# Kernel optimization log

Measured on AMD Instinct MI355X. Metric: run time of the kernel, lower is better.

The kernel has to match this reference:

```python
import jax, jax.numpy as jnp
import numpy as np

H = 16  # num_heads

def setup_inputs() -> dict:
    key = jax.random.key(0)
    ks = jax.random.split(key, 9)
    B, S, D = 4, 1024, 1024
    s = 0.02
    return {
        "x": jax.random.normal(ks[0], (B, S, D), jnp.float32),
        "Wq": jax.random.normal(ks[1], (D, D), jnp.float32) * s,
        "bq": jax.random.normal(ks[2], (D,), jnp.float32) * s,
        "Wk": jax.random.normal(ks[3], (D, D), jnp.float32) * s,
        "bk": jax.random.normal(ks[4], (D,), jnp.float32) * s,
        "Wv": jax.random.normal(ks[5], (D, D), jnp.float32) * s,
        "bv": jax.random.normal(ks[6], (D,), jnp.float32) * s,
        "Wo": jax.random.normal(ks[7], (D, D), jnp.float32) * s,
        "bo": jax.random.normal(ks[8], (D,), jnp.float32) * s,
    }

def reference(x, Wq, bq, Wk, bk, Wv, bv, Wo, bo):
    B, S, D = x.shape
    hd = D // H
    # Batched equivalent of the per-head Linear loop: project then split into heads.
    def proj(W, b):
        return (x @ W + b).reshape(B, S, H, hd).transpose(0, 2, 1, 3)  # [B,H,S,hd]
    q, k, v = proj(Wq, bq), proj(Wk, bk), proj(Wv, bv)
    scores = jnp.einsum("bhqd,bhkd->bhqk", q, k) / jnp.sqrt(jnp.float32(hd))
    probs = jax.nn.softmax(scores, axis=-1)  # [B,H,S,S] (dropout p=0 -> identity)
    ctx = jnp.einsum("bhqk,bhkd->bhqd", probs, v)  # [B,H,S,hd]
    ctx = ctx.transpose(0, 2, 1, 3).reshape(B, S, D)  # concat heads
    out = ctx @ Wo + bo
    return out, probs
```

## Files before the change

kernel.cpp:

```cpp
#include <hip/hip_runtime.h>
#include <math.h>

typedef unsigned short u16;
typedef __attribute__((ext_vector_type(8))) short short8;
typedef __attribute__((ext_vector_type(4))) float f32x4;

#define BB 4
#define SS 1024
#define DD 1024
#define NH 16
#define HD 64
#define BH 64

__device__ __forceinline__ u16 f2bf(float f) {
    union { float f; unsigned u; } v;
    v.f = f;
    unsigned r = v.u + 0x7fffu + ((v.u >> 16) & 1u);
    return (u16)(r >> 16);
}

__device__ __forceinline__ void gll16(const void* g, void* l) {
    __builtin_amdgcn_global_load_lds((__attribute__((address_space(1))) void*)g,
                                     (__attribute__((address_space(3))) void*)l, 16, 0, 0);
}

__global__ void cast_bf16(const float* __restrict__ X, u16* __restrict__ Y) {
    const int i = blockIdx.x * blockDim.x + threadIdx.x;
    const float4 v = reinterpret_cast<const float4*>(X)[i];
    ushort4 o;
    o.x = f2bf(v.x); o.y = f2bf(v.y); o.z = f2bf(v.z); o.w = f2bf(v.w);
    reinterpret_cast<ushort4*>(Y)[i] = o;
}

__global__ void transpose_cast_w(const float* __restrict__ W0, const float* __restrict__ W1,
                                 const float* __restrict__ W2, const float* __restrict__ W3,
                                 u16* __restrict__ O0, u16* __restrict__ O1,
                                 u16* __restrict__ O2, u16* __restrict__ O3) {
    __shared__ float T[64][65];
    const int z = blockIdx.z;
    const float* W = (z == 0) ? W0 : (z == 1) ? W1 : (z == 2) ? W2 : W3;
    u16* O = (z == 0) ? O0 : (z == 1) ? O1 : (z == 2) ? O2 : O3;
    const int k0 = blockIdx.x * 64, n0 = blockIdx.y * 64;
    const int x = threadIdx.x & 63, yq = threadIdx.x >> 6;
#pragma unroll
    for (int r = 0; r < 16; r++) {
        const int row = yq * 16 + r;
        T[row][x] = W[(size_t)(k0 + row) * 1024 + n0 + x];
    }
    __syncthreads();
#pragma unroll
    for (int r = 0; r < 16; r++) {
        const int row = yq * 16 + r;
        O[(size_t)(n0 + row) * 1024 + k0 + x] = f2bf(T[x][row]);
    }
}

__global__ void transpose_v(const u16* __restrict__ V, u16* __restrict__ VT) {
    __shared__ u16 T[64][66];
    const int t0 = blockIdx.x * 64;
    const size_t hbase = (size_t)blockIdx.y * (SS * HD);
    const int x = threadIdx.x & 63, yq = threadIdx.x >> 6;
#pragma unroll
    for (int r = 0; r < 16; r++) {
        const int trow = yq * 16 + r;
        T[trow][x] = V[hbase + (size_t)(t0 + trow) * 64 + x];
    }
    __syncthreads();
#pragma unroll
    for (int r = 0; r < 16; r++) {
        const int drow = yq * 16 + r;
        VT[hbase + (size_t)drow * 1024 + t0 + x] = T[x][drow];
    }
}

template <int MODE, int QKV>
__global__ __launch_bounds__(256) void mfma_gemm(
    const u16* __restrict__ A,
    const u16* __restrict__ Bt0, const u16* __restrict__ Bt1, const u16* __restrict__ Bt2,
    const float* __restrict__ bias0, const float* __restrict__ bias1, const float* __restrict__ bias2,
    void* __restrict__ out0, void* __restrict__ out1, void* __restrict__ out2) {
    __shared__ __align__(16) u16 As[128][32];
    __shared__ __align__(16) u16 Bs[128][32];

    const u16* Bt = Bt0;
    const float* bias = bias0;
    void* out = out0;
    if (QKV) {
        const int z = blockIdx.z;
        Bt = (z == 0) ? Bt0 : (z == 1) ? Bt1 : Bt2;
        bias = (z == 0) ? bias0 : (z == 1) ? bias1 : bias2;
        out = (z == 0) ? out0 : (z == 1) ? out1 : out2;
    }

    const int tid = threadIdx.x;
    const int w = tid >> 6, lane = tid & 63, l15 = lane & 15, quad = lane >> 4;
    const int wr = w >> 1, wc = w & 1;
    const int m0 = blockIdx.y * 128, n0 = blockIdx.x * 128;

    const u16* Ag = A + (size_t)(m0 + (tid >> 2)) * 1024 + (tid & 3) * 8;
    const u16* Bg = Bt + (size_t)(n0 + (tid >> 2)) * 1024 + (tid & 3) * 8;

    f32x4 acc[4][4];
#pragma unroll
    for (int i = 0; i < 4; i++)
#pragma unroll
        for (int j = 0; j < 4; j++) acc[i][j] = (f32x4){0.f, 0.f, 0.f, 0.f};

    for (int k0 = 0; k0 < 1024; k0 += 32) {
#pragma unroll
        for (int i = 0; i < 2; i++) {
            gll16(Ag + (size_t)(i * 64) * 1024 + k0, &As[i * 64 + w * 16][0]);
            gll16(Bg + (size_t)(i * 64) * 1024 + k0, &Bs[i * 64 + w * 16][0]);
        }
        __syncthreads();
        short8 af[4], bf[4];
#pragma unroll
        for (int i = 0; i < 4; i++)
            af[i] = *(const short8*)(&As[wr * 64 + i * 16 + l15][quad * 8]);
#pragma unroll
        for (int j = 0; j < 4; j++)
            bf[j] = *(const short8*)(&Bs[wc * 64 + j * 16 + l15][quad * 8]);
#pragma unroll
        for (int i = 0; i < 4; i++)
#pragma unroll
            for (int j = 0; j < 4; j++)
                acc[i][j] = __builtin_amdgcn_mfma_f32_16x16x32_bf16(af[i], bf[j], acc[i][j], 0, 0, 0);
        __syncthreads();
    }

#pragma unroll
    for (int i = 0; i < 4; i++) {
#pragma unroll
        for (int j = 0; j < 4; j++) {
            const int nn = n0 + wc * 64 + j * 16 + l15;
            const float bb = bias[nn];
#pragma unroll
            for (int r = 0; r < 4; r++) {
                const int mm = m0 + wr * 64 + i * 16 + quad * 4 + r;
                const float val = acc[i][j][r] + bb;
                if (MODE == 0) {
                    const int b = mm >> 10, s = mm & 1023, h = nn >> 6, d = nn & 63;
                    ((u16*)out)[((size_t)(b * NH + h) * SS + s) * HD + d] = f2bf(val);
                } else {
                    ((float*)out)[(size_t)mm * 1024 + nn] = val;
                }
            }
        }
    }
}

__global__ __launch_bounds__(256) void attn_fused(
    const u16* __restrict__ Qg, const u16* __restrict__ Kg, const u16* __restrict__ VTg,
    float* __restrict__ probs, u16* __restrict__ ctx) {
    __shared__ __align__(16) u16 Ks[2][2][64][32];
    __shared__ __align__(16) u16 Vs[2][2][64][32];
    __shared__ __align__(16) u16 Ps[4][2][16][32];

    const int tid = threadIdx.x;
    const int w = tid >> 6, lane = tid & 63, l15 = lane & 15, quad = lane >> 4;
    const int s0 = blockIdx.x * 64;
    const int bh = blockIdx.y;
    const size_t hbase = (size_t)bh * (SS * HD);

    const int qg = s0 + w * 16 + l15;
    const short8 bq0 = *(const short8*)(Qg + hbase + (size_t)qg * 64 + quad * 8);
    const short8 bq1 = *(const short8*)(Qg + hbase + (size_t)qg * 64 + 32 + quad * 8);

    float l_i = 0.f;
    {
        short8 akA[8], akB[8];
        auto loadK = [&](short8* ak, int kt) {
#pragma unroll
            for (int c = 0; c < 4; c++) {
                const u16* kr = Kg + hbase + (size_t)(kt * 64 + c * 16 + l15) * 64 + quad * 8;
                ak[c * 2] = *(const short8*)kr;
                ak[c * 2 + 1] = *(const short8*)(kr + 32);
            }
        };
        auto stats = [&](const short8* ak) {
            f32x4 sc[4];
#pragma unroll
            for (int c = 0; c < 4; c++) {
                f32x4 z = {0.f, 0.f, 0.f, 0.f};
                z = __builtin_amdgcn_mfma_f32_16x16x32_bf16(ak[c * 2], bq0, z, 0, 0, 0);
                z = __builtin_amdgcn_mfma_f32_16x16x32_bf16(ak[c * 2 + 1], bq1, z, 0, 0, 0);
                sc[c] = z;
            }
            float ss = 0.f;
#pragma unroll
            for (int c = 0; c < 4; c++)
#pragma unroll
                for (int r = 0; r < 4; r++) ss += __expf(sc[c][r] * 0.125f);
            ss += __shfl_xor(ss, 16);
            ss += __shfl_xor(ss, 32);
            l_i += ss;
        };
        loadK(akA, 0);
#pragma unroll 1
        for (int kt = 0; kt < 16; kt += 2) {
            loadK(akB, kt + 1);
            stats(akA);
            if (kt + 2 < 16) loadK(akA, kt + 2);
            stats(akB);
        }
    }
    const float linv = 1.0f / l_i;

    f32x4 oacc[4];
#pragma unroll
    for (int j = 0; j < 4; j++) oacc[j] = (f32x4){0.f, 0.f, 0.f, 0.f};

    const size_t prow = ((size_t)bh * SS + qg) * SS;

    auto stage = [&](int buf, int kt) {
#pragma unroll
        for (int i = 0; i < 2; i++) {
            const int c = i * 256 + tid;
            const int ks = c >> 8, row = (c >> 2) & 63, ch = c & 3;
            const int cb = i * 256 + (tid & ~63);
            gll16(Kg + hbase + (size_t)(kt * 64 + row) * 64 + ks * 32 + ch * 8,
                  &Ks[buf][0][0][0] + (size_t)cb * 8);
            gll16(VTg + hbase + (size_t)row * 1024 + kt * 64 + ks * 32 + ch * 8,
                  &Vs[buf][0][0][0] + (size_t)cb * 8);
        }
    };

    stage(0, 0);
    asm volatile("s_waitcnt vmcnt(0)" ::: "memory");
    __builtin_amdgcn_s_barrier();

#pragma unroll 1
    for (int kt = 0; kt < 16; kt++) {
        const int cur = kt & 1;
        if (kt < 15) stage(cur ^ 1, kt + 1);

        f32x4 sc[4];
#pragma unroll
        for (int c = 0; c < 4; c++) {
            const short8 ak0 = *(const short8*)(&Ks[cur][0][c * 16 + l15][quad * 8]);
            const short8 ak1 = *(const short8*)(&Ks[cur][1][c * 16 + l15][quad * 8]);
            f32x4 z = {0.f, 0.f, 0.f, 0.f};
            z = __builtin_amdgcn_mfma_f32_16x16x32_bf16(ak0, bq0, z, 0, 0, 0);
            z = __builtin_amdgcn_mfma_f32_16x16x32_bf16(ak1, bq1, z, 0, 0, 0);
            sc[c] = z;
        }
#pragma unroll
        for (int c = 0; c < 4; c++) {
            float p[4];
            f32x4 pv;
#pragma unroll
            for (int r = 0; r < 4; r++) {
                p[r] = __expf(sc[c][r] * 0.125f) * linv;
                pv[r] = p[r];
            }
            *(f32x4*)(probs + prow + kt * 64 + c * 16 + quad * 4) = pv;
            uint2 pk;
            pk.x = (unsigned)f2bf(p[0]) | ((unsigned)f2bf(p[1]) << 16);
            pk.y = (unsigned)f2bf(p[2]) | ((unsigned)f2bf(p[3]) << 16);
            *(uint2*)(&Ps[w][c >> 1][l15][(c & 1) * 16 + quad * 4]) = pk;
        }
        const short8 ap0 = *(const short8*)(&Ps[w][0][l15][quad * 8]);
        const short8 ap1 = *(const short8*)(&Ps[w][1][l15][quad * 8]);
#pragma unroll
        for (int j = 0; j < 4; j++) {
            const short8 bv0 = *(const short8*)(&Vs[cur][0][j * 16 + l15][quad * 8]);
            const short8 bv1 = *(const short8*)(&Vs[cur][1][j * 16 + l15][quad * 8]);
            oacc[j] = __builtin_amdgcn_mfma_f32_16x16x32_bf16(ap0, bv0, oacc[j], 0, 0, 0);
            oacc[j] = __builtin_amdgcn_mfma_f32_16x16x32_bf16(ap1, bv1, oacc[j], 0, 0, 0);
        }
        asm volatile("s_waitcnt vmcnt(0)" ::: "memory");
        __builtin_amdgcn_s_barrier();
    }

    const int b = bh >> 4, h = bh & 15;
#pragma unroll
    for (int j = 0; j < 4; j++)
#pragma unroll
        for (int r = 0; r < 4; r++) {
            const int s = s0 + w * 16 + quad * 4 + r;
            ctx[((size_t)b * SS + s) * DD + h * HD + j * 16 + l15] = f2bf(oacc[j][r]);
        }
}

extern "C" void kernel_launch(void* const* d_in, const int* in_sizes, int n_in,
                              void* d_out, int out_size, void* d_ws, size_t ws_size,
                              hipStream_t stream) {
    const float* x  = (const float*)d_in[0];
    const float* Wq = (const float*)d_in[1];
    const float* bq = (const float*)d_in[2];
    const float* Wk = (const float*)d_in[3];
    const float* bk = (const float*)d_in[4];
    const float* Wv = (const float*)d_in[5];
    const float* bv = (const float*)d_in[6];
    const float* Wo = (const float*)d_in[7];
    const float* bo = (const float*)d_in[8];

    float* out   = (float*)d_out;
    float* probs = out + (size_t)BB * SS * DD;

    char* ws = (char*)d_ws;
    u16* xb   = (u16*)(ws);
    u16* Wtq  = (u16*)(ws + (8ull << 20));
    u16* Wtk  = (u16*)(ws + (10ull << 20));
    u16* Wtv  = (u16*)(ws + (12ull << 20));
    u16* Wto  = (u16*)(ws + (14ull << 20));
    u16* qb   = (u16*)(ws + (16ull << 20));
    u16* kb   = (u16*)(ws + (24ull << 20));
    u16* vb   = (u16*)(ws + (32ull << 20));
    u16* vTb  = (u16*)(ws + (40ull << 20));
    u16* ctxb = (u16*)(ws + (48ull << 20));

    const dim3 blk(256);

    cast_bf16<<<dim3(4096), blk, 0, stream>>>(x, xb);
    transpose_cast_w<<<dim3(16, 16, 4), blk, 0, stream>>>(Wq, Wk, Wv, Wo, Wtq, Wtk, Wtv, Wto);

    mfma_gemm<0, 1><<<dim3(8, 32, 3), blk, 0, stream>>>(
        xb, Wtq, Wtk, Wtv, bq, bk, bv, qb, kb, vb);

    transpose_v<<<dim3(16, 64), blk, 0, stream>>>(vb, vTb);

    attn_fused<<<dim3(16, 64), blk, 0, stream>>>(qb, kb, vTb, probs, ctxb);

    mfma_gemm<1, 0><<<dim3(8, 32), blk, 0, stream>>>(
        ctxb, Wto, nullptr, nullptr, bo, nullptr, nullptr, out, nullptr, nullptr);
}
```

Measured before the change: 488.3 us.

## Narrow GEMM tiles, LDS-staged softmax stats pass, setprio around MFMA

```diff
diff --git a/kernel.cpp b/kernel.cpp
--- a/kernel.cpp
+++ b/kernel.cpp
@@ -80,7 +80,7 @@
     const float* __restrict__ bias0, const float* __restrict__ bias1, const float* __restrict__ bias2,
     void* __restrict__ out0, void* __restrict__ out1, void* __restrict__ out2) {
     __shared__ __align__(16) u16 As[128][32];
-    __shared__ __align__(16) u16 Bs[128][32];
+    __shared__ __align__(16) u16 Bs[64][32];
 
     const u16* Bt = Bt0;
     const float* bias = bias0;
@@ -95,44 +95,48 @@
     const int tid = threadIdx.x;
     const int w = tid >> 6, lane = tid & 63, l15 = lane & 15, quad = lane >> 4;
     const int wr = w >> 1, wc = w & 1;
-    const int m0 = blockIdx.y * 128, n0 = blockIdx.x * 128;
-
-    const u16* Ag = A + (size_t)(m0 + (tid >> 2)) * 1024 + (tid & 3) * 8;
-    const u16* Bg = Bt + (size_t)(n0 + (tid >> 2)) * 1024 + (tid & 3) * 8;
-
-    f32x4 acc[4][4];
+    const int m0 = blockIdx.y * 128, n0 = blockIdx.x * 64;
+
+    f32x4 acc[4][2];
 #pragma unroll
     for (int i = 0; i < 4; i++)
 #pragma unroll
-        for (int j = 0; j < 4; j++) acc[i][j] = (f32x4){0.f, 0.f, 0.f, 0.f};
-
+        for (int j = 0; j < 2; j++) acc[i][j] = (f32x4){0.f, 0.f, 0.f, 0.f};
+
+    const int srow = tid >> 2, sch = tid & 3;
     for (int k0 = 0; k0 < 1024; k0 += 32) {
 #pragma unroll
         for (int i = 0; i < 2; i++) {
-            gll16(Ag + (size_t)(i * 64) * 1024 + k0, &As[i * 64 + w * 16][0]);
-            gll16(Bg + (size_t)(i * 64) * 1024 + k0, &Bs[i * 64 + w * 16][0]);
-        }
+            const int c = i * 256 + tid;
+            const int row = c >> 2, ch = c & 3;
+            const int cb = i * 256 + (tid & ~63);
+            gll16(A + (size_t)(m0 + row) * 1024 + k0 + ch * 8, &As[0][0] + (size_t)cb * 8);
+        }
+        gll16(Bt + (size_t)(n0 + srow) * 1024 + k0 + sch * 8,
+              &Bs[0][0] + (size_t)(tid & ~63) * 8);
         __syncthreads();
-        short8 af[4], bf[4];
+        short8 af[4], bf[2];
 #pragma unroll
         for (int i = 0; i < 4; i++)
             af[i] = *(const short8*)(&As[wr * 64 + i * 16 + l15][quad * 8]);
 #pragma unroll
-        for (int j = 0; j < 4; j++)
-            bf[j] = *(const short8*)(&Bs[wc * 64 + j * 16 + l15][quad * 8]);
+        for (int j = 0; j < 2; j++)
+            bf[j] = *(const short8*)(&Bs[wc * 32 + j * 16 + l15][quad * 8]);
+        __builtin_amdgcn_s_setprio(1);
 #pragma unroll
         for (int i = 0; i < 4; i++)
 #pragma unroll
-            for (int j = 0; j < 4; j++)
+            for (int j = 0; j < 2; j++)
                 acc[i][j] = __builtin_amdgcn_mfma_f32_16x16x32_bf16(af[i], bf[j], acc[i][j], 0, 0, 0);
+        __builtin_amdgcn_s_setprio(0);
         __syncthreads();
     }
 
 #pragma unroll
     for (int i = 0; i < 4; i++) {
 #pragma unroll
-        for (int j = 0; j < 4; j++) {
-            const int nn = n0 + wc * 64 + j * 16 + l15;
+        for (int j = 0; j < 2; j++) {
+            const int nn = n0 + wc * 32 + j * 16 + l15;
             const float bb = bias[nn];
 #pragma unroll
             for (int r = 0; r < 4; r++) {
@@ -166,53 +170,8 @@
     const short8 bq0 = *(const short8*)(Qg + hbase + (size_t)qg * 64 + quad * 8);
     const short8 bq1 = *(const short8*)(Qg + hbase + (size_t)qg * 64 + 32 + quad * 8);
 
-    float l_i = 0.f;
-    {
-        short8 akA[8], akB[8];
-        auto loadK = [&](short8* ak, int kt) {
-#pragma unroll
-            for (int c = 0; c < 4; c++) {
-                const u16* kr = Kg + hbase + (size_t)(kt * 64 + c * 16 + l15) * 64 + quad * 8;
-                ak[c * 2] = *(const short8*)kr;
-                ak[c * 2 + 1] = *(const short8*)(kr + 32);
-            }
-        };
-        auto stats = [&](const short8* ak) {
-            f32x4 sc[4];
-#pragma unroll
-            for (int c = 0; c < 4; c++) {
-                f32x4 z = {0.f, 0.f, 0.f, 0.f};
-                z = __builtin_amdgcn_mfma_f32_16x16x32_bf16(ak[c * 2], bq0, z, 0, 0, 0);
-                z = __builtin_amdgcn_mfma_f32_16x16x32_bf16(ak[c * 2 + 1], bq1, z, 0, 0, 0);
-                sc[c] = z;
-            }
-            float ss = 0.f;
-#pragma unroll
-            for (int c = 0; c < 4; c++)
-#pragma unroll
-                for (int r = 0; r < 4; r++) ss += __expf(sc[c][r] * 0.125f);
-            ss += __shfl_xor(ss, 16);
-            ss += __shfl_xor(ss, 32);
-            l_i += ss;
-        };
-        loadK(akA, 0);
-#pragma unroll 1
-        for (int kt = 0; kt < 16; kt += 2) {
-            loadK(akB, kt + 1);
-            stats(akA);
-            if (kt + 2 < 16) loadK(akA, kt + 2);
-            stats(akB);
-        }
-    }
-    const float linv = 1.0f / l_i;
-
-    f32x4 oacc[4];
-#pragma unroll
-    for (int j = 0; j < 4; j++) oacc[j] = (f32x4){0.f, 0.f, 0.f, 0.f};
-
-    const size_t prow = ((size_t)bh * SS + qg) * SS;
-
-    auto stage = [&](int buf, int kt) {
+    const int sks = tid >> 6 >= 0 ? 0 : 0;
+    auto stageK = [&](int buf, int kt) {
 #pragma unroll
         for (int i = 0; i < 2; i++) {
             const int c = i * 256 + tid;
@@ -220,21 +179,64 @@
             const int cb = i * 256 + (tid & ~63);
             gll16(Kg + hbase + (size_t)(kt * 64 + row) * 64 + ks * 32 + ch * 8,
                   &Ks[buf][0][0][0] + (size_t)cb * 8);
+        }
+    };
+    auto stageV = [&](int buf, int kt) {
+#pragma unroll
+        for (int i = 0; i < 2; i++) {
+            const int c = i * 256 + tid;
+            const int ks = c >> 8, row = (c >> 2) & 63, ch = c & 3;
+            const int cb = i * 256 + (tid & ~63);
             gll16(VTg + hbase + (size_t)row * 1024 + kt * 64 + ks * 32 + ch * 8,
                   &Vs[buf][0][0][0] + (size_t)cb * 8);
         }
     };
 
-    stage(0, 0);
+    float l_i = 0.f;
+    stageK(0, 0);
     asm volatile("s_waitcnt vmcnt(0)" ::: "memory");
     __builtin_amdgcn_s_barrier();
-
 #pragma unroll 1
     for (int kt = 0; kt < 16; kt++) {
         const int cur = kt & 1;
-        if (kt < 15) stage(cur ^ 1, kt + 1);
+        if (kt < 15) stageK(cur ^ 1, kt + 1);
+        float ss = 0.f;
+#pragma unroll
+        for (int c = 0; c < 4; c++) {
+            const short8 ak0 = *(const short8*)(&Ks[cur][0][c * 16 + l15][quad * 8]);
+            const short8 ak1 = *(const short8*)(&Ks[cur][1][c * 16 + l15][quad * 8]);
+            f32x4 z = {0.f, 0.f, 0.f, 0.f};
+            z = __builtin_amdgcn_mfma_f32_16x16x32_bf16(ak0, bq0, z, 0, 0, 0);
+            z = __builtin_amdgcn_mfma_f32_16x16x32_bf16(ak1, bq1, z, 0, 0, 0);
+#pragma unroll
+            for (int r = 0; r < 4; r++) ss += __expf(z[r] * 0.125f);
+        }
+        ss += __shfl_xor(ss, 16);
+        ss += __shfl_xor(ss, 32);
+        l_i += ss;
+        asm volatile("s_waitcnt vmcnt(0)" ::: "memory");
+        __builtin_amdgcn_s_barrier();
+    }
+    const float nlog = -__logf(l_i);
+
+    f32x4 oacc[4];
+#pragma unroll
+    for (int j = 0; j < 4; j++) oacc[j] = (f32x4){0.f, 0.f, 0.f, 0.f};
+
+    const size_t prow = ((size_t)bh * SS + qg) * SS;
+
+    stageK(0, 0);
+    stageV(0, 0);
+    asm volatile("s_waitcnt vmcnt(0)" ::: "memory");
+    __builtin_amdgcn_s_barrier();
+
+#pragma unroll 1
+    for (int kt = 0; kt < 16; kt++) {
+        const int cur = kt & 1;
+        if (kt < 15) { stageK(cur ^ 1, kt + 1); stageV(cur ^ 1, kt + 1); }
 
         f32x4 sc[4];
+        __builtin_amdgcn_s_setprio(1);
 #pragma unroll
         for (int c = 0; c < 4; c++) {
             const short8 ak0 = *(const short8*)(&Ks[cur][0][c * 16 + l15][quad * 8]);
@@ -244,13 +246,14 @@
             z = __builtin_amdgcn_mfma_f32_16x16x32_bf16(ak1, bq1, z, 0, 0, 0);
             sc[c] = z;
         }
+        __builtin_amdgcn_s_setprio(0);
 #pragma unroll
         for (int c = 0; c < 4; c++) {
             float p[4];
             f32x4 pv;
 #pragma unroll
             for (int r = 0; r < 4; r++) {
-                p[r] = __expf(sc[c][r] * 0.125f) * linv;
+                p[r] = __expf(fmaf(sc[c][r], 0.125f, nlog));
                 pv[r] = p[r];
             }
             *(f32x4*)(probs + prow + kt * 64 + c * 16 + quad * 4) = pv;
@@ -261,6 +264,7 @@
         }
         const short8 ap0 = *(const short8*)(&Ps[w][0][l15][quad * 8]);
         const short8 ap1 = *(const short8*)(&Ps[w][1][l15][quad * 8]);
+        __builtin_amdgcn_s_setprio(1);
 #pragma unroll
         for (int j = 0; j < 4; j++) {
             const short8 bv0 = *(const short8*)(&Vs[cur][0][j * 16 + l15][quad * 8]);
@@ -268,6 +272,7 @@
             oacc[j] = __builtin_amdgcn_mfma_f32_16x16x32_bf16(ap0, bv0, oacc[j], 0, 0, 0);
             oacc[j] = __builtin_amdgcn_mfma_f32_16x16x32_bf16(ap1, bv1, oacc[j], 0, 0, 0);
         }
+        __builtin_amdgcn_s_setprio(0);
         asm volatile("s_waitcnt vmcnt(0)" ::: "memory");
         __builtin_amdgcn_s_barrier();
     }
@@ -315,13 +320,13 @@
     cast_bf16<<<dim3(4096), blk, 0, stream>>>(x, xb);
     transpose_cast_w<<<dim3(16, 16, 4), blk, 0, stream>>>(Wq, Wk, Wv, Wo, Wtq, Wtk, Wtv, Wto);
 
-    mfma_gemm<0, 1><<<dim3(8, 32, 3), blk, 0, stream>>>(
+    mfma_gemm<0, 1><<<dim3(16, 32, 3), blk, 0, stream>>>(
         xb, Wtq, Wtk, Wtv, bq, bk, bv, qb, kb, vb);
 
     transpose_v<<<dim3(16, 64), blk, 0, stream>>>(vb, vTb);
 
     attn_fused<<<dim3(16, 64), blk, 0, stream>>>(qb, kb, vTb, probs, ctxb);
 
-    mfma_gemm<1, 0><<<dim3(8, 32), blk, 0, stream>>>(
+    mfma_gemm<1, 0><<<dim3(16, 32), blk, 0, stream>>>(
         ctxb, Wto, nullptr, nullptr, bo, nullptr, nullptr, out, nullptr, nullptr);
 }
```

After: 439.7 us. -9.9%, faster.
